# Performance work log

Hardware: AMD Instinct MI355X
Metric: run time of the kernel (lower is better)

Reference implementation:

```python
import jax, jax.numpy as jnp
import numpy as np
from jax import lax

B, H, W = 16, 256, 256
NUM_HIDDEN = 12
C = 3 + NUM_HIDDEN + 1  # 16 channels: rgb + hidden + alpha
HID = 64
ALPHA = 1.0
THR = 0.1

SOBEL_X = jnp.array([[-1.0, 0.0, 1.0], [-2.0, 0.0, 2.0], [-1.0, 0.0, 1.0]], jnp.float32) / 8.0
SOBEL_Y = jnp.array([[-1.0, -2.0, -1.0], [0.0, 0.0, 0.0], [1.0, 2.0, 1.0]], jnp.float32) / 8.0


def _sobel_conv(s, k):
    # s: [B,H,W] channel-summed state; k: [3,3]. SAME-padded 2D stencil.
    return lax.conv_general_dilated(
        s[..., None], k[:, :, None, None], window_strides=(1, 1), padding='SAME',
        dimension_numbers=('NHWC', 'HWIO', 'NHWC'))  # [B,H,W,1]


def _alive(x, thr):
    # 3x3 max-pool over alpha channel (index 3), SAME padding.
    a = x[..., 3:4]
    pooled = lax.reduce_window(a, -jnp.inf, lax.max, (1, 3, 3, 1), (1, 1, 1, 1), 'SAME')
    return pooled > thr  # [B,H,W,1] bool


def setup_inputs() -> dict:
    key = jax.random.key(0)
    ks = jax.random.split(key, 7)
    x = jax.random.uniform(ks[0], (B, H, W, C), dtype=jnp.float32)
    # UpdateNet params: 1x1 convs stored as dense matrices [in, out].
    w1 = jax.random.normal(ks[1], (3 * C, HID), dtype=jnp.float32) * (1.0 / np.sqrt(3 * C))
    b1 = jnp.zeros((HID,), jnp.float32)
    w2 = jax.random.normal(ks[2], (HID, HID), dtype=jnp.float32) * (1.0 / np.sqrt(HID))
    b2 = jnp.zeros((HID,), jnp.float32)
    # Original zero-inits w3; use small random values so outputs/grads are nontrivial.
    w3 = jax.random.normal(ks[3], (HID, C), dtype=jnp.float32) * 0.01
    return {'x': x, 'w1': w1, 'b1': b1, 'w2': w2, 'b2': b2, 'w3': w3}


def reference(x, w1, b1, w2, b2, w3):
    pre_life = _alive(x, THR)
    # Sobel perception: kernel[o,i] = sobel for all o,i  =>  each output channel
    # is the sobel filter applied to the channel-sum; broadcast across C channels.
    s = jnp.sum(x, axis=-1)                      # [B,H,W]
    sx = _sobel_conv(s, SOBEL_X)                 # [B,H,W,1]
    sy = _sobel_conv(s, SOBEL_Y)                 # [B,H,W,1]
    perc = jnp.concatenate(
        [x, jnp.broadcast_to(sx, x.shape), jnp.broadcast_to(sy, x.shape)], axis=-1)  # [B,H,W,3C]
    # UpdateNet: two biased 1x1 convs + ReLU, then unbiased 1x1 conv.
    h = jax.nn.relu(jnp.einsum('bhwi,io->bhwo', perc, w1) + b1)
    h = jax.nn.relu(jnp.einsum('bhwi,io->bhwo', h, w2) + b2)
    update = jnp.einsum('bhwi,io->bhwo', h, w3)  # [B,H,W,C]
    # cell_fire_rate == 1.0 -> stochastic update mask is all ones.
    x_new = x + ALPHA * update
    post_life = _alive(x_new, THR)
    life = (pre_life & post_life).astype(x_new.dtype)
    return x_new * life
```

## Files before the change

### kernel.cpp

```cpp
#include <hip/hip_runtime.h>
#include <hip/hip_bf16.h>
#include <cstdint>

#define NPIX (16 * 256 * 256)
#define THRV 0.1f

typedef __bf16 bf16x8 __attribute__((ext_vector_type(8)));
typedef float  f32x4  __attribute__((ext_vector_type(4)));

#define NSLOT 18

__global__ __launch_bounds__(64) void k_pack(const float* __restrict__ w1,
                                             const float* __restrict__ b1,
                                             const float* __restrict__ w2,
                                             const float* __restrict__ b2,
                                             const float* __restrict__ w3,
                                             float4* __restrict__ wpack) {
    const int lane = threadIdx.x;
    const int r = lane & 15, g = lane >> 4;
#pragma unroll
    for (int n = 0; n < 4; ++n) {
        const int cc = n * 16 + r;
        bf16x8 f;
#pragma unroll
        for (int j = 0; j < 8; ++j) {
            float v = 0.f;
            if (j < 4) v = w1[(g * 4 + j) * 64 + cc];
            else if (g == 0 && j == 4) { for (int t = 0; t < 16; ++t) v += w1[(16 + t) * 64 + cc]; v *= 0.125f; }
            else if (g == 0 && j == 5) { for (int t = 0; t < 16; ++t) v += w1[(32 + t) * 64 + cc]; v *= 0.125f; }
            else if (g == 1 && j == 4) v = b1[cc];
            f[j] = (__bf16)v;
        }
        wpack[n * 64 + lane] = *(const float4*)&f;
    }
#pragma unroll
    for (int s = 0; s < 2; ++s)
#pragma unroll
        for (int n = 0; n < 4; ++n) {
            bf16x8 f;
#pragma unroll
            for (int j = 0; j < 8; ++j) {
                const int psi = (2 * s + (j >> 2)) * 16 + g * 4 + (j & 3);
                f[j] = (__bf16)w2[psi * 64 + n * 16 + r];
            }
            wpack[(4 + s * 4 + n) * 64 + lane] = *(const float4*)&f;
        }
#pragma unroll
    for (int s = 0; s < 2; ++s) {
        bf16x8 f;
#pragma unroll
        for (int j = 0; j < 8; ++j) {
            const int psi = (2 * s + (j >> 2)) * 16 + g * 4 + (j & 3);
            f[j] = (__bf16)w3[psi * 16 + r];
        }
        wpack[(12 + s) * 64 + lane] = *(const float4*)&f;
    }
#pragma unroll
    for (int n = 0; n < 4; ++n) {
        f32x4 v;
#pragma unroll
        for (int q = 0; q < 4; ++q) v[q] = b2[n * 16 + g * 4 + q];
        wpack[(14 + n) * 64 + lane] = *(const float4*)&v;
    }
}

__global__ __launch_bounds__(256, 3) void k_fused(const float* __restrict__ x,
                                                  const float4* __restrict__ wpack,
                                                  float* __restrict__ out,
                                                  unsigned char* __restrict__ rpre,
                                                  unsigned char* __restrict__ anewf) {
    __shared__ float sS[4][256];
    __shared__ float sC3[2][256];

    const int tid = threadIdx.x;
    const int wv = tid >> 6, lane = tid & 63;
    const int r = lane & 15, g = lane >> 4;

    bf16x8 w1f[4], w2f[2][4], w3f[2];
    f32x4 b2v[4];
#pragma unroll
    for (int n = 0; n < 4; ++n) { float4 t = wpack[n * 64 + lane]; w1f[n] = *(bf16x8*)&t; }
#pragma unroll
    for (int s2i = 0; s2i < 2; ++s2i)
#pragma unroll
        for (int n = 0; n < 4; ++n) { float4 t = wpack[(4 + s2i * 4 + n) * 64 + lane]; w2f[s2i][n] = *(bf16x8*)&t; }
#pragma unroll
    for (int s2i = 0; s2i < 2; ++s2i) { float4 t = wpack[(12 + s2i) * 64 + lane]; w3f[s2i] = *(bf16x8*)&t; }
#pragma unroll
    for (int n = 0; n < 4; ++n) { float4 t = wpack[(14 + n) * 64 + lane]; b2v[n] = *(f32x4*)&t; }

    const int pair = (blockIdx.x & 7) * 256 + (blockIdx.x >> 3);
    const int y0row = pair * 2;
    const int y = y0row & 255;
    const size_t rbase0 = (size_t)y0row * 256;
    const bool ymok = (y > 0), ypok = (y < 254);

    float hs0 = 0.f, hs1 = 0.f;
    if (ymok) {
        const float4* pm = (const float4*)(x + (rbase0 - 256 + tid) * 16);
        float4 a = pm[0], b = pm[1], c = pm[2], d = pm[3];
        hs0 = ((a.x + a.y) + (a.z + a.w)) + ((b.x + b.y) + (b.z + b.w)) +
              ((c.x + c.y) + (c.z + c.w)) + ((d.x + d.y) + (d.z + d.w));
    }
    if (ypok) {
        const float4* pp = (const float4*)(x + (rbase0 + 512 + tid) * 16);
        float4 a = pp[0], b = pp[1], c = pp[2], d = pp[3];
        hs1 = ((a.x + a.y) + (a.z + a.w)) + ((b.x + b.y) + (b.z + b.w)) +
              ((c.x + c.y) + (c.z + c.w)) + ((d.x + d.y) + (d.z + d.w));
    }
    sS[0][tid] = hs0;
    sS[3][tid] = hs1;

    const int rowi = wv >> 1;
    const int colbase = (wv & 1) * 128;
    const size_t rb = rbase0 + (size_t)rowi * 256;

    float4 xf[8];
#pragma unroll
    for (int t = 0; t < 8; ++t) {
        const int col = colbase + t * 16 + r;
        xf[t] = *(const float4*)(x + (rb + col) * 16 + g * 4);
        float p = (xf[t].x + xf[t].y) + (xf[t].z + xf[t].w);
        p += __shfl_xor(p, 16);
        p += __shfl_xor(p, 32);
        if (g == 0) { sS[1 + rowi][col] = p; sC3[rowi][col] = xf[t].w; }
    }
    __syncthreads();

#pragma unroll
    for (int t = 0; t < 8; ++t) {
        const int col = colbase + t * 16 + r;
        const size_t pix = rb + col;
        const bool cl = (col > 0), cr = (col < 255);

        const float r0m = cl ? sS[rowi][col - 1] : 0.f;
        const float r0c = sS[rowi][col];
        const float r0p = cr ? sS[rowi][col + 1] : 0.f;
        const float r1m = cl ? sS[rowi + 1][col - 1] : 0.f;
        const float r1p = cr ? sS[rowi + 1][col + 1] : 0.f;
        const float r2m = cl ? sS[rowi + 2][col - 1] : 0.f;
        const float r2c = sS[rowi + 2][col];
        const float r2p = cr ? sS[rowi + 2][col + 1] : 0.f;
        const float gx = (r0p - r0m) + 2.f * (r1p - r1m) + (r2p - r2m);
        const float gy = (r2m + 2.f * r2c + r2p) - (r0m + 2.f * r0c + r0p);

        if (g == 0) {
            const float c3m = cl ? sC3[rowi][col - 1] : 0.f;
            const float c3c = sC3[rowi][col];
            const float c3p = cr ? sC3[rowi][col + 1] : 0.f;
            rpre[pix] = (fmaxf(c3m, fmaxf(c3c, c3p)) > THRV) ? 1 : 0;
        }

        bf16x8 a1;
        a1[0] = (__bf16)xf[t].x; a1[1] = (__bf16)xf[t].y;
        a1[2] = (__bf16)xf[t].z; a1[3] = (__bf16)xf[t].w;
        a1[4] = (__bf16)(g == 0 ? gx : (g == 1 ? 1.f : 0.f));
        a1[5] = (__bf16)(g == 0 ? gy : 0.f);
        a1[6] = (__bf16)0.f; a1[7] = (__bf16)0.f;

        f32x4 acc1[4];
#pragma unroll
        for (int n = 0; n < 4; ++n)
            acc1[n] = __builtin_amdgcn_mfma_f32_16x16x32_bf16(
                w1f[n], a1, (f32x4){0.f, 0.f, 0.f, 0.f}, 0, 0, 0);

        bf16x8 bf2[2];
#pragma unroll
        for (int s2i = 0; s2i < 2; ++s2i)
#pragma unroll
            for (int j = 0; j < 4; ++j) {
                bf2[s2i][j]     = (__bf16)fmaxf(acc1[2 * s2i][j], 0.f);
                bf2[s2i][4 + j] = (__bf16)fmaxf(acc1[2 * s2i + 1][j], 0.f);
            }

        f32x4 acc2[4];
#pragma unroll
        for (int n = 0; n < 4; ++n) {
            acc2[n] = __builtin_amdgcn_mfma_f32_16x16x32_bf16(w2f[0][n], bf2[0], b2v[n], 0, 0, 0);
            acc2[n] = __builtin_amdgcn_mfma_f32_16x16x32_bf16(w2f[1][n], bf2[1], acc2[n], 0, 0, 0);
        }

        bf16x8 bf3[2];
#pragma unroll
        for (int s2i = 0; s2i < 2; ++s2i)
#pragma unroll
            for (int j = 0; j < 4; ++j) {
                bf3[s2i][j]     = (__bf16)fmaxf(acc2[2 * s2i][j], 0.f);
                bf3[s2i][4 + j] = (__bf16)fmaxf(acc2[2 * s2i + 1][j], 0.f);
            }

        f32x4 acc3 = __builtin_amdgcn_mfma_f32_16x16x32_bf16(
            w3f[0], bf3[0], (f32x4){0.f, 0.f, 0.f, 0.f}, 0, 0, 0);
        acc3 = __builtin_amdgcn_mfma_f32_16x16x32_bf16(w3f[1], bf3[1], acc3, 0, 0, 0);

        f32x4 xn;
        xn[0] = xf[t].x + acc3[0]; xn[1] = xf[t].y + acc3[1];
        xn[2] = xf[t].z + acc3[2]; xn[3] = xf[t].w + acc3[3];
        __builtin_nontemporal_store(xn, (f32x4*)(out + pix * 16 + g * 4));
        if (g == 0) anewf[pix] = (xn[3] > THRV) ? 1 : 0;
    }
}

__global__ __launch_bounds__(256) void k_post(const unsigned char* __restrict__ rpre,
                                              const unsigned char* __restrict__ anewf,
                                              float* __restrict__ out) {
    const int q = blockIdx.x * 256 + threadIdx.x;
    const int p0 = q * 4;
    const int bi = p0 >> 16;
    const int rem = p0 & 65535;
    const int y = rem >> 8;
    const int c0 = rem & 255;
    const unsigned char* pr = rpre + ((size_t)bi << 16);
    const unsigned char* an = anewf + ((size_t)bi << 16);

    unsigned pre = 0, M = 0, l = 0, rr = 0;
#pragma unroll
    for (int dy = -1; dy <= 1; ++dy) {
        const int y2 = y + dy;
        if ((unsigned)y2 >= 256u) continue;
        const int ro = y2 * 256;
        pre |= *(const unsigned*)(pr + ro + c0);
        M   |= *(const unsigned*)(an + ro + c0);
        l   |= (c0 > 0)   ? (unsigned)an[ro + c0 - 1] : 0u;
        rr  |= (c0 < 252) ? (unsigned)an[ro + c0 + 4] : 0u;
    }
    const unsigned post = M | (M << 8) | l | (M >> 8) | (rr << 24);
    const unsigned alive = pre & post;
    if (alive != 0x01010101u) {
        const f32x4 z = (f32x4){0.f, 0.f, 0.f, 0.f};
#pragma unroll
        for (int i = 0; i < 4; ++i)
            if (!((alive >> (8 * i)) & 1u)) {
                f32x4* op = (f32x4*)(out + (size_t)(p0 + i) * 16);
                op[0] = z; op[1] = z; op[2] = z; op[3] = z;
            }
    }
}

extern "C" void kernel_launch(void* const* d_in, const int* in_sizes, int n_in,
                              void* d_out, int out_size, void* d_ws, size_t ws_size,
                              hipStream_t stream) {
    const float* x  = (const float*)d_in[0];
    const float* w1 = (const float*)d_in[1];
    const float* b1 = (const float*)d_in[2];
    const float* w2 = (const float*)d_in[3];
    const float* b2 = (const float*)d_in[4];
    const float* w3 = (const float*)d_in[5];
    float* out = (float*)d_out;

    unsigned char* rpre  = (unsigned char*)d_ws;
    unsigned char* anewf = rpre + NPIX;
    float4* wpack = (float4*)(anewf + NPIX);

    hipLaunchKernelGGL(k_pack, dim3(1), dim3(64), 0, stream, w1, b1, w2, b2, w3, wpack);
    hipLaunchKernelGGL(k_fused, dim3(NPIX / 512), dim3(256), 0, stream,
                       x, wpack, out, rpre, anewf);
    hipLaunchKernelGGL(k_post, dim3(NPIX / 1024), dim3(256), 0, stream,
                       rpre, anewf, out);
}
```

Baseline: 46.64 us.

## Stream 8-row strips per block with rolling row buffer and prefetch

```diff
diff --git a/kernel.cpp b/kernel.cpp
--- a/kernel.cpp
+++ b/kernel.cpp
@@ -64,13 +64,13 @@
     }
 }
 
-__global__ __launch_bounds__(256, 3) void k_fused(const float* __restrict__ x,
+__global__ __launch_bounds__(256, 2) void k_fused(const float* __restrict__ x,
                                                   const float4* __restrict__ wpack,
                                                   float* __restrict__ out,
                                                   unsigned char* __restrict__ rpre,
                                                   unsigned char* __restrict__ anewf) {
     __shared__ float sS[4][256];
-    __shared__ float sC3[2][256];
+    __shared__ float sC3[4][256];
 
     const int tid = threadIdx.x;
     const int wv = tid >> 6, lane = tid & 63;
@@ -89,115 +89,132 @@
 #pragma unroll
     for (int n = 0; n < 4; ++n) { float4 t = wpack[(14 + n) * 64 + lane]; b2v[n] = *(f32x4*)&t; }
 
-    const int pair = (blockIdx.x & 7) * 256 + (blockIdx.x >> 3);
-    const int y0row = pair * 2;
-    const int y = y0row & 255;
-    const size_t rbase0 = (size_t)y0row * 256;
-    const bool ymok = (y > 0), ypok = (y < 254);
-
-    float hs0 = 0.f, hs1 = 0.f;
-    if (ymok) {
-        const float4* pm = (const float4*)(x + (rbase0 - 256 + tid) * 16);
-        float4 a = pm[0], b = pm[1], c = pm[2], d = pm[3];
-        hs0 = ((a.x + a.y) + (a.z + a.w)) + ((b.x + b.y) + (b.z + b.w)) +
-              ((c.x + c.y) + (c.z + c.w)) + ((d.x + d.y) + (d.z + d.w));
-    }
-    if (ypok) {
-        const float4* pp = (const float4*)(x + (rbase0 + 512 + tid) * 16);
-        float4 a = pp[0], b = pp[1], c = pp[2], d = pp[3];
-        hs1 = ((a.x + a.y) + (a.z + a.w)) + ((b.x + b.y) + (b.z + b.w)) +
-              ((c.x + c.y) + (c.z + c.w)) + ((d.x + d.y) + (d.z + d.w));
-    }
-    sS[0][tid] = hs0;
-    sS[3][tid] = hs1;
-
-    const int rowi = wv >> 1;
-    const int colbase = (wv & 1) * 128;
-    const size_t rb = rbase0 + (size_t)rowi * 256;
-
-    float4 xf[8];
-#pragma unroll
-    for (int t = 0; t < 8; ++t) {
-        const int col = colbase + t * 16 + r;
-        xf[t] = *(const float4*)(x + (rb + col) * 16 + g * 4);
-        float p = (xf[t].x + xf[t].y) + (xf[t].z + xf[t].w);
-        p += __shfl_xor(p, 16);
-        p += __shfl_xor(p, 32);
-        if (g == 0) { sS[1 + rowi][col] = p; sC3[rowi][col] = xf[t].w; }
-    }
-    __syncthreads();
-
-#pragma unroll
-    for (int t = 0; t < 8; ++t) {
-        const int col = colbase + t * 16 + r;
-        const size_t pix = rb + col;
-        const bool cl = (col > 0), cr = (col < 255);
-
-        const float r0m = cl ? sS[rowi][col - 1] : 0.f;
-        const float r0c = sS[rowi][col];
-        const float r0p = cr ? sS[rowi][col + 1] : 0.f;
-        const float r1m = cl ? sS[rowi + 1][col - 1] : 0.f;
-        const float r1p = cr ? sS[rowi + 1][col + 1] : 0.f;
-        const float r2m = cl ? sS[rowi + 2][col - 1] : 0.f;
-        const float r2c = sS[rowi + 2][col];
-        const float r2p = cr ? sS[rowi + 2][col + 1] : 0.f;
-        const float gx = (r0p - r0m) + 2.f * (r1p - r1m) + (r2p - r2m);
-        const float gy = (r2m + 2.f * r2c + r2p) - (r0m + 2.f * r0c + r0p);
-
-        if (g == 0) {
-            const float c3m = cl ? sC3[rowi][col - 1] : 0.f;
-            const float c3c = sC3[rowi][col];
-            const float c3p = cr ? sC3[rowi][col + 1] : 0.f;
-            rpre[pix] = (fmaxf(c3m, fmaxf(c3c, c3p)) > THRV) ? 1 : 0;
-        }
-
-        bf16x8 a1;
-        a1[0] = (__bf16)xf[t].x; a1[1] = (__bf16)xf[t].y;
-        a1[2] = (__bf16)xf[t].z; a1[3] = (__bf16)xf[t].w;
-        a1[4] = (__bf16)(g == 0 ? gx : (g == 1 ? 1.f : 0.f));
-        a1[5] = (__bf16)(g == 0 ? gy : 0.f);
-        a1[6] = (__bf16)0.f; a1[7] = (__bf16)0.f;
-
-        f32x4 acc1[4];
-#pragma unroll
-        for (int n = 0; n < 4; ++n)
-            acc1[n] = __builtin_amdgcn_mfma_f32_16x16x32_bf16(
-                w1f[n], a1, (f32x4){0.f, 0.f, 0.f, 0.f}, 0, 0, 0);
-
-        bf16x8 bf2[2];
-#pragma unroll
-        for (int s2i = 0; s2i < 2; ++s2i)
-#pragma unroll
-            for (int j = 0; j < 4; ++j) {
-                bf2[s2i][j]     = (__bf16)fmaxf(acc1[2 * s2i][j], 0.f);
-                bf2[s2i][4 + j] = (__bf16)fmaxf(acc1[2 * s2i + 1][j], 0.f);
-            }
-
-        f32x4 acc2[4];
-#pragma unroll
-        for (int n = 0; n < 4; ++n) {
-            acc2[n] = __builtin_amdgcn_mfma_f32_16x16x32_bf16(w2f[0][n], bf2[0], b2v[n], 0, 0, 0);
-            acc2[n] = __builtin_amdgcn_mfma_f32_16x16x32_bf16(w2f[1][n], bf2[1], acc2[n], 0, 0, 0);
-        }
-
-        bf16x8 bf3[2];
-#pragma unroll
-        for (int s2i = 0; s2i < 2; ++s2i)
-#pragma unroll
-            for (int j = 0; j < 4; ++j) {
-                bf3[s2i][j]     = (__bf16)fmaxf(acc2[2 * s2i][j], 0.f);
-                bf3[s2i][4 + j] = (__bf16)fmaxf(acc2[2 * s2i + 1][j], 0.f);
-            }
-
-        f32x4 acc3 = __builtin_amdgcn_mfma_f32_16x16x32_bf16(
-            w3f[0], bf3[0], (f32x4){0.f, 0.f, 0.f, 0.f}, 0, 0, 0);
-        acc3 = __builtin_amdgcn_mfma_f32_16x16x32_bf16(w3f[1], bf3[1], acc3, 0, 0, 0);
-
-        f32x4 xn;
-        xn[0] = xf[t].x + acc3[0]; xn[1] = xf[t].y + acc3[1];
-        xn[2] = xf[t].z + acc3[2]; xn[3] = xf[t].w + acc3[3];
-        __builtin_nontemporal_store(xn, (f32x4*)(out + pix * 16 + g * 4));
-        if (g == 0) anewf[pix] = (xn[3] > THRV) ? 1 : 0;
+    const int swz = (blockIdx.x & 7) * 64 + (blockIdx.x >> 3);
+    const int img = swz >> 5;
+    const int y0 = (swz & 31) * 8;
+    const size_t ibase = (size_t)img << 16;
+    const int wcol = wv * 64;
+
+    float4 xf[4], xfA[4], xfN[4];
+
+    auto loadrow = [&](int yl, float4 dst[4]) {
+        if ((unsigned)yl < 256u) {
+            const size_t rb = ibase + (size_t)yl * 256;
+#pragma unroll
+            for (int t = 0; t < 4; ++t)
+                dst[t] = *(const float4*)(x + (rb + wcol + t * 16 + r) * 16 + g * 4);
+        } else {
+#pragma unroll
+            for (int t = 0; t < 4; ++t) dst[t] = make_float4(0.f, 0.f, 0.f, 0.f);
+        }
+    };
+    auto redwrite = [&](int yl, const float4 src[4]) {
+        const int sl = yl & 3;
+#pragma unroll
+        for (int t = 0; t < 4; ++t) {
+            float p = (src[t].x + src[t].y) + (src[t].z + src[t].w);
+            p += __shfl_xor(p, 16);
+            p += __shfl_xor(p, 32);
+            if (g == 0) { sS[sl][wcol + t * 16 + r] = p; sC3[sl][wcol + t * 16 + r] = src[t].w; }
+        }
+    };
+
+    loadrow(y0 - 1, xfN);
+    loadrow(y0, xf);
+    loadrow(y0 + 1, xfA);
+    redwrite(y0 - 1, xfN);
+    redwrite(y0, xf);
+
+#pragma unroll 1
+    for (int p = 0; p < 8; ++p) {
+        const int y = y0 + p;
+
+        const int yn = (p < 7) ? (y + 2) : 999;
+        loadrow(yn, xfN);
+
+        redwrite(y + 1, xfA);
+        __syncthreads();
+
+        const float* s0 = sS[(y - 1) & 3];
+        const float* s1 = sS[y & 3];
+        const float* s2 = sS[(y + 1) & 3];
+        const float* c3 = sC3[y & 3];
+        const size_t rb = ibase + (size_t)y * 256;
+#pragma unroll
+        for (int t = 0; t < 4; ++t) {
+            const int col = wcol + t * 16 + r;
+            const size_t pix = rb + col;
+            const bool cl = (col > 0), cr = (col < 255);
+
+            const float r0m = cl ? s0[col - 1] : 0.f;
+            const float r0c = s0[col];
+            const float r0p = cr ? s0[col + 1] : 0.f;
+            const float r1m = cl ? s1[col - 1] : 0.f;
+            const float r1p = cr ? s1[col + 1] : 0.f;
+            const float r2m = cl ? s2[col - 1] : 0.f;
+            const float r2c = s2[col];
+            const float r2p = cr ? s2[col + 1] : 0.f;
+            const float gx = (r0p - r0m) + 2.f * (r1p - r1m) + (r2p - r2m);
+            const float gy = (r2m + 2.f * r2c + r2p) - (r0m + 2.f * r0c + r0p);
+
+            if (g == 0) {
+                const float c3m = cl ? c3[col - 1] : 0.f;
+                const float c3c = c3[col];
+                const float c3p = cr ? c3[col + 1] : 0.f;
+                rpre[pix] = (fmaxf(c3m, fmaxf(c3c, c3p)) > THRV) ? 1 : 0;
+            }
+
+            bf16x8 a1;
+            a1[0] = (__bf16)xf[t].x; a1[1] = (__bf16)xf[t].y;
+            a1[2] = (__bf16)xf[t].z; a1[3] = (__bf16)xf[t].w;
+            a1[4] = (__bf16)(g == 0 ? gx : (g == 1 ? 1.f : 0.f));
+            a1[5] = (__bf16)(g == 0 ? gy : 0.f);
+            a1[6] = (__bf16)0.f; a1[7] = (__bf16)0.f;
+
+            f32x4 acc1[4];
+#pragma unroll
+            for (int n = 0; n < 4; ++n)
+                acc1[n] = __builtin_amdgcn_mfma_f32_16x16x32_bf16(
+                    w1f[n], a1, (f32x4){0.f, 0.f, 0.f, 0.f}, 0, 0, 0);
+
+            bf16x8 bf2[2];
+#pragma unroll
+            for (int s2i = 0; s2i < 2; ++s2i)
+#pragma unroll
+                for (int j = 0; j < 4; ++j) {
+                    bf2[s2i][j]     = (__bf16)fmaxf(acc1[2 * s2i][j], 0.f);
+                    bf2[s2i][4 + j] = (__bf16)fmaxf(acc1[2 * s2i + 1][j], 0.f);
+                }
+
+            f32x4 acc2[4];
+#pragma unroll
+            for (int n = 0; n < 4; ++n) {
+                acc2[n] = __builtin_amdgcn_mfma_f32_16x16x32_bf16(w2f[0][n], bf2[0], b2v[n], 0, 0, 0);
+                acc2[n] = __builtin_amdgcn_mfma_f32_16x16x32_bf16(w2f[1][n], bf2[1], acc2[n], 0, 0, 0);
+            }
+
+            bf16x8 bf3[2];
+#pragma unroll
+            for (int s2i = 0; s2i < 2; ++s2i)
+#pragma unroll
+                for (int j = 0; j < 4; ++j) {
+                    bf3[s2i][j]     = (__bf16)fmaxf(acc2[2 * s2i][j], 0.f);
+                    bf3[s2i][4 + j] = (__bf16)fmaxf(acc2[2 * s2i + 1][j], 0.f);
+                }
+
+            f32x4 acc3 = __builtin_amdgcn_mfma_f32_16x16x32_bf16(
+                w3f[0], bf3[0], (f32x4){0.f, 0.f, 0.f, 0.f}, 0, 0, 0);
+            acc3 = __builtin_amdgcn_mfma_f32_16x16x32_bf16(w3f[1], bf3[1], acc3, 0, 0, 0);
+
+            f32x4 xn;
+            xn[0] = xf[t].x + acc3[0]; xn[1] = xf[t].y + acc3[1];
+            xn[2] = xf[t].z + acc3[2]; xn[3] = xf[t].w + acc3[3];
+            __builtin_nontemporal_store(xn, (f32x4*)(out + pix * 16 + g * 4));
+            if (g == 0) anewf[pix] = (xn[3] > THRV) ? 1 : 0;
+        }
+
+#pragma unroll
+        for (int t = 0; t < 4; ++t) { xf[t] = xfA[t]; xfA[t] = xfN[t]; }
     }
 }
 
@@ -253,7 +270,7 @@
     float4* wpack = (float4*)(anewf + NPIX);
 
     hipLaunchKernelGGL(k_pack, dim3(1), dim3(64), 0, stream, w1, b1, w2, b2, w3, wpack);
-    hipLaunchKernelGGL(k_fused, dim3(NPIX / 512), dim3(256), 0, stream,
+    hipLaunchKernelGGL(k_fused, dim3(512), dim3(256), 0, stream,
                        x, wpack, out, rpre, anewf);
     hipLaunchKernelGGL(k_post, dim3(NPIX / 1024), dim3(256), 0, stream,
                        rpre, anewf, out);
```

After: 45.11 us. -3.3%, faster.
